# Kernel optimization log

Hardware: AMD Instinct MI355X
Metric: run time of the kernel (lower is better)

The kernel has to match this reference:

```python
import jax, jax.numpy as jnp
import numpy as np

N_NODES = 50000
N_EDGES = 800000
LN_EPS = 1e-5


def _segment_softmax_aggr(msg, t, dst, n):
    # SoftmaxAggregation(learn=True): alpha = softmax(msg * t) per dest segment, out = sum(alpha * msg)
    logits = msg * t  # [E, C]
    m = jax.ops.segment_max(logits, dst, num_segments=n)
    m = jnp.where(jnp.isfinite(m), m, 0.0)  # empty segments -> 0 to keep exp finite
    e = jnp.exp(logits - m[dst])
    denom = jax.ops.segment_sum(e, dst, num_segments=n)
    alpha = e / jnp.maximum(denom[dst], 1e-16)
    return jax.ops.segment_sum(alpha * msg, dst, num_segments=n)


def _sage_conv(x, src, dst, wp, bp, t, wl, bl, wr):
    # project=True: messages come from relu(lin(x)); root term uses ORIGINAL x
    xp = jax.nn.relu(x @ wp + bp)
    msg = xp[src]                                   # [E, C] gather
    aggr = _segment_softmax_aggr(msg, t, dst, x.shape[0])
    out = aggr @ wl + bl + x @ wr
    # normalize=True: L2 normalize rows (eps as in F.normalize)
    nrm = jnp.maximum(jnp.linalg.norm(out, axis=-1, keepdims=True), 1e-12)
    return out / nrm


def _mem_pool(x, k, w_conv, wl, bl):
    # PyG MemPooling, tau=1: Student-t kernel 1/(1+d^2)
    H, K, F = k.shape
    kk = k.reshape(H * K, F)
    d2 = (jnp.sum(kk * kk, -1)[:, None] + jnp.sum(x * x, -1)[None, :]
          - 2.0 * kk @ x.T)                          # [H*K, N]
    d2 = jnp.maximum(d2, 0.0)
    dist = 1.0 / (1.0 + d2)
    dist = dist.reshape(H, K, -1).transpose(0, 2, 1)  # [H, N, K]
    S = dist / jnp.sum(dist, -1, keepdims=True)       # per-head normalize over clusters
    S = jnp.einsum('h,hnk->nk', w_conv, S)            # 1x1 conv mixing heads (no bias)
    S = jax.nn.softmax(S, axis=-1)                    # [N, K]
    xp = S.T @ x                                      # [K, F]
    return xp @ wl + bl                               # [K, out]


def setup_inputs() -> dict:
    key = jax.random.key(0)
    ks = jax.random.split(key, 20)
    rn = lambda i, shp, s: jax.random.normal(ks[i], shp, dtype=jnp.float32) * s
    inp = {
        'x': rn(0, (N_NODES, 64), 1.0),
        'edge_index': jax.random.randint(ks[1], (2, N_EDGES), 0, N_NODES, dtype=jnp.int32),
        'w_proj1': rn(2, (64, 64), 0.1), 'b_proj1': rn(3, (64,), 0.05),
        't1': jnp.ones((64,), jnp.float32),
        'w_l1': rn(4, (64, 256), 0.1), 'b_l1': rn(5, (256,), 0.05),
        'w_r1': rn(6, (64, 256), 0.1),
        'w_proj2': rn(7, (256, 256), 0.05), 'b_proj2': rn(8, (256,), 0.05),
        't2': jnp.ones((256,), jnp.float32),
        'w_l2': rn(9, (256, 128), 0.05), 'b_l2': rn(10, (128,), 0.05),
        'w_r2': rn(11, (256, 128), 0.05),
        'k_mem': rn(12, (4, 4, 128), 1.0),
        'w_conv': rn(13, (4,), 0.5),
        'w_memlin': rn(14, (128, 128), 0.08), 'b_memlin': rn(15, (128,), 0.05),
        'w_fx': rn(16, (128, 64), 0.08), 'b_fx': rn(17, (64,), 0.05),
        'gamma': jnp.ones((64,), jnp.float32),
        'beta': jnp.zeros((64,), jnp.float32),
    }
    return inp


def reference(x, edge_index, w_proj1, b_proj1, t1, w_l1, b_l1, w_r1,
              w_proj2, b_proj2, t2, w_l2, b_l2, w_r2,
              k_mem, w_conv, w_memlin, b_memlin, w_fx, b_fx, gamma, beta):
    src, dst = edge_index[0], edge_index[1]
    h = _sage_conv(x, src, dst, w_proj1, b_proj1, t1, w_l1, b_l1, w_r1)
    h = jax.nn.relu(h)                              # dropout = identity (eval)
    h = _sage_conv(h, src, dst, w_proj2, b_proj2, t2, w_l2, b_l2, w_r2)
    h = jax.nn.relu(h)
    pooled = _mem_pool(h, k_mem, w_conv, w_memlin, b_memlin)  # [4, 128]
    g = jnp.mean(pooled, axis=0, keepdims=True)     # global_mean_pool -> [1, 128]
    y = g @ w_fx + b_fx                             # [1, 64]
    mu = jnp.mean(y, -1, keepdims=True)
    var = jnp.var(y, -1, keepdims=True)
    y = (y - mu) / jnp.sqrt(var + LN_EPS) * gamma + beta
    return jax.nn.relu(y)
```

## Files before the change

kernel.cpp:

```cpp
#include <hip/hip_runtime.h>
#include <hip/hip_bf16.h>

#define N_NODES 50000
#define N_EDGES 800000
#define NB 196
#define PC_SLICES 2048

typedef __attribute__((ext_vector_type(8))) short short8;
typedef __attribute__((ext_vector_type(4))) float f32x4;
typedef __attribute__((ext_vector_type(2))) float f32x2;

#define QSCALE2 (2.f / 255.f)
#define QINV2   127.5f
#define QSCALE1 (12.75f / 255.f)
#define QINV1   20.f

__device__ __forceinline__ float us2f(unsigned short u) {
    return __uint_as_float(((unsigned int)u) << 16);
}
__device__ __forceinline__ unsigned short f2bu(float f) {
    unsigned int u = __float_as_uint(f);
    unsigned int r = (u + 0x7fffu + ((u >> 16) & 1u)) >> 16;
    return (unsigned short)r;
}
__device__ __forceinline__ float exp2_hw(float x) {
    float r;
    __asm__("v_exp_f32 %0, %1" : "=v"(r) : "v"(x));
    return r;
}
#define LOG2E 1.44269504088896f

__global__ void k_hist(const int* __restrict__ dst, int* __restrict__ counts) {
    int e = blockIdx.x * 256 + threadIdx.x;
    if (e < N_EDGES) atomicAdd(&counts[dst[e]], 1);
}

__global__ __launch_bounds__(256) void k_scan1(const int* __restrict__ counts,
                                               int* __restrict__ row_ptr,
                                               int* __restrict__ partial) {
    __shared__ int sd[256];
    int t = threadIdx.x, i = blockIdx.x * 256 + t;
    int v = (i < N_NODES) ? counts[i] : 0;
    sd[t] = v;
    __syncthreads();
    for (int off = 1; off < 256; off <<= 1) {
        int o = (t >= off) ? sd[t - off] : 0;
        __syncthreads();
        sd[t] += o;
        __syncthreads();
    }
    if (i < N_NODES) row_ptr[i] = sd[t] - v;
    if (t == 255) partial[blockIdx.x] = sd[255];
}

__global__ __launch_bounds__(256) void k_scan3b(int* __restrict__ row_ptr,
                                                const int* __restrict__ partial,
                                                int* __restrict__ cursor) {
    __shared__ int sd[256];
    int t = threadIdx.x;
    sd[t] = (t < blockIdx.x) ? partial[t] : 0;
    __syncthreads();
    for (int off = 128; off > 0; off >>= 1) {
        if (t < off) sd[t] += sd[t + off];
        __syncthreads();
    }
    int base = sd[0];
    int i = blockIdx.x * 256 + t;
    if (i < N_NODES) {
        int v = row_ptr[i] + base;
        row_ptr[i] = v;
        cursor[i] = v;
    }
    if (blockIdx.x == 0 && t == 0) row_ptr[N_NODES] = N_EDGES;
}

__global__ void k_scatter(const int* __restrict__ src, const int* __restrict__ dst,
                          int* __restrict__ cursor, int* __restrict__ src_sorted) {
    int e = blockIdx.x * 256 + threadIdx.x;
    if (e < N_EDGES) {
        int d = dst[e];
        int pos = atomicAdd(&cursor[d], 1);
        src_sorted[pos] = src[e];
    }
}

#define XCAST_N (N_NODES * 64)
__global__ __launch_bounds__(256) void k_prep(const float* __restrict__ x,
                                              const float* __restrict__ wp1,
                                              const float* __restrict__ wl1,
                                              const float* __restrict__ wr1,
                                              const float* __restrict__ wp2,
                                              const float* __restrict__ wl2,
                                              const float* __restrict__ wr2,
                                              unsigned short* __restrict__ cat1,
                                              unsigned short* __restrict__ B0T,
                                              unsigned short* __restrict__ B1T,
                                              unsigned short* __restrict__ BP2T,
                                              unsigned short* __restrict__ B2T) {
    int idx = blockIdx.x * 256 + threadIdx.x;
    if (idx < XCAST_N) {
        int i = idx >> 6, j = idx & 63;
        cat1[i * 128 + 64 + j] = f2bu(x[idx]);
        return;
    }
    int w = idx - XCAST_N;
    if (w < 4096)  { int k = w >> 6, n = w & 63;  B0T[n * 64 + k] = f2bu(wp1[w]); return; }
    w -= 4096;
    if (w < 16384) { int k = w >> 8, n = w & 255; B1T[n * 128 + k] = f2bu(wl1[w]); return; }
    w -= 16384;
    if (w < 16384) { int k = w >> 8, n = w & 255; B1T[n * 128 + 64 + k] = f2bu(wr1[w]); return; }
    w -= 16384;
    if (w < 65536) { int k = w >> 8, n = w & 255; BP2T[n * 256 + k] = f2bu(wp2[w]); return; }
    w -= 65536;
    if (w < 32768) { int k = w >> 7, n = w & 127; B2T[n * 512 + k] = f2bu(wl2[w]); return; }
    w -= 32768;
    if (w < 32768) { int k = w >> 7, n = w & 127; B2T[n * 512 + 256 + k] = f2bu(wr2[w]); return; }
}

template<int K, int C, int LDA, int LDOUT, int OUT_OFF, int EP, int WPB>
__global__ __launch_bounds__(256, WPB) void k_gemm(const unsigned short* __restrict__ A,
                                                   const unsigned short* __restrict__ BT,
                                                   const float* __restrict__ bias,
                                                   void* __restrict__ outv,
                                                   const float* __restrict__ kmem,
                                                   const float* __restrict__ wconv,
                                                   float* __restrict__ Sm,
                                                   float qinv) {
    constexpr int NT = C / 16;
    constexpr int SAE = 128 * 72;
    constexpr int SBE = C * 72;
    constexpr int STAGE_B = (SAE + SBE) * 2;
    constexpr int RP_B = 64 * C * (EP == 2 ? 4 : (EP == 3 ? 1 : 2));
    constexpr int SMEM_B = STAGE_B > RP_B ? STAGE_B : RP_B;
    constexpr int POOL_B = (EP == 2) ? (2048 * 4 + 64 + 16) : 16;
    __shared__ __align__(16) char smem[SMEM_B + POOL_B];
    unsigned short* sA = (unsigned short*)smem;
    unsigned short* sB = sA + SAE;
    float* kls  = (float*)(smem + SMEM_B);
    float* kk2s = kls + 2048;
    float* wcs  = kk2s + 16;

    int t = threadIdx.x;
    int wid = t >> 6, lane = t & 63;
    int lrow = lane & 15, quad = lane >> 4;
    int m0 = blockIdx.x * 128;

    if (EP == 2) {
        for (int i = t; i < 2048; i += 256) kls[i] = kmem[i];
        if (t < 4) wcs[t] = wconv[t];
        __syncthreads();
        if (t < 16) {
            float s = 0.f;
            for (int f = 0; f < 128; ++f) { float v = kls[t * 128 + f]; s += v * v; }
            kk2s[t] = s;
        }
    }

    f32x4 acc[2][NT];
#pragma unroll
    for (int h = 0; h < 2; ++h)
#pragma unroll
        for (int nt = 0; nt < NT; ++nt)
#pragma unroll
            for (int r = 0; r < 4; ++r) acc[h][nt][r] = 0.f;

    for (int k0 = 0; k0 < K; k0 += 64) {
        __syncthreads();
        for (int i = t; i < 1024; i += 256) {
            int r = i >> 3, seg = i & 7;
            int m = m0 + r;
            uint4 v = make_uint4(0u, 0u, 0u, 0u);
            if (m < N_NODES) v = *(const uint4*)&A[(size_t)m * LDA + k0 + seg * 8];
            *(uint4*)&sA[r * 72 + seg * 8] = v;
        }
        for (int i = t; i < C * 8; i += 256) {
            int n = i >> 3, seg = i & 7;
            uint4 v = *(const uint4*)&BT[(size_t)n * K + k0 + seg * 8];
            *(uint4*)&sB[n * 72 + seg * 8] = v;
        }
        __syncthreads();
#pragma unroll
        for (int kk = 0; kk < 2; ++kk) {
            short8 a0 = *(const short8*)&sA[(wid * 16 + lrow) * 72 + kk * 32 + quad * 8];
            short8 a1 = *(const short8*)&sA[(64 + wid * 16 + lrow) * 72 + kk * 32 + quad * 8];
#pragma unroll
            for (int nt = 0; nt < NT; ++nt) {
                short8 bfg = *(const short8*)&sB[(nt * 16 + lrow) * 72 + kk * 32 + quad * 8];
                acc[0][nt] = __builtin_amdgcn_mfma_f32_16x16x32_bf16(a0, bfg, acc[0][nt], 0, 0, 0);
                acc[1][nt] = __builtin_amdgcn_mfma_f32_16x16x32_bf16(a1, bfg, acc[1][nt], 0, 0, 0);
            }
        }
    }

#pragma unroll
    for (int h = 0; h < 2; ++h) {
#pragma unroll
        for (int nt = 0; nt < NT; ++nt) {
            float bv = bias[nt * 16 + lrow];
#pragma unroll
            for (int r = 0; r < 4; ++r) acc[h][nt][r] += bv;
        }
        if (EP == 1 || EP == 2) {
#pragma unroll
            for (int r = 0; r < 4; ++r) {
                float ss = 0.f;
#pragma unroll
                for (int nt = 0; nt < NT; ++nt) ss += acc[h][nt][r] * acc[h][nt][r];
                ss += __shfl_xor(ss, 1);
                ss += __shfl_xor(ss, 2);
                ss += __shfl_xor(ss, 4);
                ss += __shfl_xor(ss, 8);
                float rinv = 1.f / fmaxf(sqrtf(ss), 1e-12f);
#pragma unroll
                for (int nt = 0; nt < NT; ++nt)
                    acc[h][nt][r] = fmaxf(acc[h][nt][r] * rinv, 0.f);
            }
        } else {
#pragma unroll
            for (int nt = 0; nt < NT; ++nt)
#pragma unroll
                for (int r = 0; r < 4; ++r) acc[h][nt][r] = fmaxf(acc[h][nt][r], 0.f);
        }
    }

    __syncthreads();
#pragma unroll
    for (int h = 0; h < 2; ++h) {
        if (EP == 2) {
            float* rp = (float*)smem;
#pragma unroll
            for (int nt = 0; nt < NT; ++nt)
#pragma unroll
                for (int r = 0; r < 4; ++r)
                    rp[(wid * 16 + quad * 4 + r) * C + nt * 16 + lrow] = acc[h][nt][r];
            __syncthreads();
            float* outp = (float*)outv;
            for (int i = t; i < 64 * C / 4; i += 256) {
                int f = i * 4, r = f / C, c = f % C;
                int m = m0 + h * 64 + r;
                if (m < N_NODES)
                    *(float4*)&outp[(size_t)m * LDOUT + OUT_OFF + c] = *(const float4*)&rp[f];
            }
            {
                int row = t >> 2, p = t & 3;
                int cbase = p * 32;
                float dots[16];
#pragma unroll
                for (int k = 0; k < 16; ++k) dots[k] = 0.f;
                float x2 = 0.f;
#pragma unroll
                for (int c4 = 0; c4 < 8; ++c4) {
                    float4 xv = *(const float4*)&rp[row * C + cbase + c4 * 4];
                    x2 += xv.x * xv.x + xv.y * xv.y + xv.z * xv.z + xv.w * xv.w;
#pragma unroll
                    for (int k = 0; k < 16; ++k) {
                        float4 kv = *(const float4*)&kls[k * 128 + cbase + c4 * 4];
                        dots[k] += xv.x * kv.x + xv.y * kv.y + xv.z * kv.z + xv.w * kv.w;
                    }
                }
#pragma unroll
                for (int k = 0; k < 16; ++k) {
                    dots[k] += __shfl_xor(dots[k], 1);
                    dots[k] += __shfl_xor(dots[k], 2);
                }
                x2 += __shfl_xor(x2, 1);
                x2 += __shfl_xor(x2, 2);
                if (p == 0) {
                    int m = m0 + h * 64 + row;
                    if (m < N_NODES) {
                        float dist[16];
#pragma unroll
                        for (int k = 0; k < 16; ++k) {
                            float d2 = fmaxf(kk2s[k] + x2 - 2.f * dots[k], 0.f);
                            dist[k] = 1.f / (1.f + d2);
                        }
                        float s0 = 0.f, s1 = 0.f, s2 = 0.f, s3 = 0.f;
#pragma unroll
                        for (int hh = 0; hh < 4; ++hh) {
                            float den = dist[hh * 4] + dist[hh * 4 + 1] +
                                        dist[hh * 4 + 2] + dist[hh * 4 + 3];
                            float inv = wcs[hh] / den;
                            s0 += dist[hh * 4 + 0] * inv;
                            s1 += dist[hh * 4 + 1] * inv;
                            s2 += dist[hh * 4 + 2] * inv;
                            s3 += dist[hh * 4 + 3] * inv;
                        }
                        float mx = fmaxf(fmaxf(s0, s1), fmaxf(s2, s3));
                        float e0 = __expf(s0 - mx), e1 = __expf(s1 - mx);
                        float e2 = __expf(s2 - mx), e3 = __expf(s3 - mx);
                        float inv = 1.f / (e0 + e1 + e2 + e3);
                        *(float4*)&Sm[(size_t)m * 4] =
                            make_float4(e0 * inv, e1 * inv, e2 * inv, e3 * inv);
                    }
                }
            }
            __syncthreads();
        } else if (EP == 3) {
            unsigned char* rp = (unsigned char*)smem;
#pragma unroll
            for (int nt = 0; nt < NT; ++nt)
#pragma unroll
                for (int r = 0; r < 4; ++r) {
                    float q = fminf(__builtin_rintf(acc[h][nt][r] * qinv), 255.f);
                    rp[(wid * 16 + quad * 4 + r) * C + nt * 16 + lrow] = (unsigned char)(int)q;
                }
            __syncthreads();
            unsigned char* outp = (unsigned char*)outv;
            for (int i = t; i < 64 * C / 16; i += 256) {
                int f = i * 16, r = f / C, c = f % C;
                int m = m0 + h * 64 + r;
                if (m < N_NODES)
                    *(uint4*)&outp[(size_t)m * LDOUT + OUT_OFF + c] = *(const uint4*)&rp[f];
            }
            __syncthreads();
        } else {
            unsigned short* rp = (unsigned short*)smem;
#pragma unroll
            for (int nt = 0; nt < NT; ++nt)
#pragma unroll
                for (int r = 0; r < 4; ++r)
                    rp[(wid * 16 + quad * 4 + r) * C + nt * 16 + lrow] = f2bu(acc[h][nt][r]);
            __syncthreads();
            unsigned short* outp = (unsigned short*)outv;
            for (int i = t; i < 64 * C / 8; i += 256) {
                int f = i * 8, r = f / C, c = f % C;
                int m = m0 + h * 64 + r;
                if (m < N_NODES)
                    *(uint4*)&outp[(size_t)m * LDOUT + OUT_OFF + c] = *(const uint4*)&rp[f];
            }
            __syncthreads();
        }
    }
}

__global__ __launch_bounds__(256) void k_aggr256(const unsigned char* __restrict__ xp,
                                                 const float* __restrict__ tvec,
                                                 const int* __restrict__ row_ptr,
                                                 const int* __restrict__ srcs,
                                                 unsigned short* __restrict__ outp) {
    int t = threadIdx.x & 63;
    int wid = threadIdx.x >> 6;
    int n = blockIdx.x * 4 + wid;
    float4 tv4 = *(const float4*)&tvec[t * 4];
    f32x2 tv01 = {tv4.x * (LOG2E * QSCALE2), tv4.y * (LOG2E * QSCALE2)};
    f32x2 tv23 = {tv4.z * (LOG2E * QSCALE2), tv4.w * (LOG2E * QSCALE2)};
    int beg = __builtin_amdgcn_readfirstlane(row_ptr[n]);
    int end = __builtin_amdgcn_readfirstlane(row_ptr[n + 1]);
    f32x2 se01 = {0.f, 0.f}, se23 = {0.f, 0.f};
    f32x2 sem01 = {0.f, 0.f}, sem23 = {0.f, 0.f};
    int e = beg;
#define EDGE_BODY(VV, MSK)                                                     \
    {                                                                          \
        f32x2 m01 = {(float)((VV) & 0xFFu), (float)(((VV) >> 8) & 0xFFu)};     \
        f32x2 m23 = {(float)(((VV) >> 16) & 0xFFu), (float)((VV) >> 24)};      \
        f32x2 l01 = m01 * tv01, l23 = m23 * tv23;                              \
        f32x2 w01, w23;                                                        \
        w01.x = exp2_hw(l01.x) * (MSK); w01.y = exp2_hw(l01.y) * (MSK);        \
        w23.x = exp2_hw(l23.x) * (MSK); w23.y = exp2_hw(l23.y) * (MSK);        \
        se01 += w01; se23 += w23;                                              \
        sem01 = __builtin_elementwise_fma(w01, m01, sem01);                    \
        sem23 = __builtin_elementwise_fma(w23, m23, sem23);                    \
    }
    for (; e + 16 <= end; e += 16) {
        unsigned int v[16];
#pragma unroll
        for (int j = 0; j < 16; ++j) {
            const unsigned char* p = xp + (size_t)srcs[e + j] * 256;
            v[j] = *(const unsigned int*)&p[t * 4];
        }
#pragma unroll
        for (int j = 0; j < 16; ++j) EDGE_BODY(v[j], 1.f)
    }
    for (; e + 8 <= end; e += 8) {
        unsigned int v[8];
#pragma unroll
        for (int j = 0; j < 8; ++j) {
            const unsigned char* p = xp + (size_t)srcs[e + j] * 256;
            v[j] = *(const unsigned int*)&p[t * 4];
        }
#pragma unroll
        for (int j = 0; j < 8; ++j) EDGE_BODY(v[j], 1.f)
    }
    if (e < end) {
        int last = end - 1;
        unsigned int v[8];
#pragma unroll
        for (int j = 0; j < 8; ++j) {
            int ee = e + j;
            ee = ee < end ? ee : last;
            const unsigned char* p = xp + (size_t)srcs[ee] * 256;
            v[j] = *(const unsigned int*)&p[t * 4];
        }
#pragma unroll
        for (int j = 0; j < 8; ++j) {
            float msk = (e + j < end) ? 1.f : 0.f;
            EDGE_BODY(v[j], msk)
        }
    }
#undef EDGE_BODY
    ushort4 o;
    o.x = f2bu(QSCALE2 * sem01.x / fmaxf(se01.x, 1e-16f));
    o.y = f2bu(QSCALE2 * sem01.y / fmaxf(se01.y, 1e-16f));
    o.z = f2bu(QSCALE2 * sem23.x / fmaxf(se23.x, 1e-16f));
    o.w = f2bu(QSCALE2 * sem23.y / fmaxf(se23.y, 1e-16f));
    *(ushort4*)&outp[(size_t)n * 512 + t * 4] = o;
}

__global__ __launch_bounds__(256) void k_aggr64(const unsigned char* __restrict__ xp,
                                                const float* __restrict__ tvec,
                                                const int* __restrict__ row_ptr,
                                                const int* __restrict__ srcs,
                                                unsigned short* __restrict__ outp) {
    int c = threadIdx.x & 63;
    int wid = threadIdx.x >> 6;
    int n = blockIdx.x * 4 + wid;
    float tv = tvec[c] * (LOG2E * QSCALE1);
    int beg = __builtin_amdgcn_readfirstlane(row_ptr[n]);
    int end = __builtin_amdgcn_readfirstlane(row_ptr[n + 1]);
    float se = 0.f, sem = 0.f;
    int e = beg;
    for (; e + 16 <= end; e += 16) {
        unsigned char v[16];
#pragma unroll
        for (int j = 0; j < 16; ++j)
            v[j] = xp[(size_t)srcs[e + j] * 64 + c];
#pragma unroll
        for (int j = 0; j < 16; ++j) {
            float msg = (float)v[j];
            float w = exp2_hw(msg * tv);
            se += w;
            sem = fmaf(w, msg, sem);
        }
    }
    for (; e + 8 <= end; e += 8) {
        unsigned char v[8];
#pragma unroll
        for (int j = 0; j < 8; ++j)
            v[j] = xp[(size_t)srcs[e + j] * 64 + c];
#pragma unroll
        for (int j = 0; j < 8; ++j) {
            float msg = (float)v[j];
            float w = exp2_hw(msg * tv);
            se += w;
            sem = fmaf(w, msg, sem);
        }
    }
    if (e < end) {
        int last = end - 1;
        unsigned char v[8];
#pragma unroll
        for (int j = 0; j < 8; ++j) {
            int ee = e + j;
            ee = ee < end ? ee : last;
            v[j] = xp[(size_t)srcs[ee] * 64 + c];
        }
#pragma unroll
        for (int j = 0; j < 8; ++j) {
            float msk = (e + j < end) ? 1.f : 0.f;
            float msg = (float)v[j];
            float w = exp2_hw(msg * tv) * msk;
            se += w;
            sem = fmaf(w, msg, sem);
        }
    }
    outp[(size_t)n * 128 + c] = f2bu(QSCALE1 * sem / fmaxf(se, 1e-16f));
}

__global__ __launch_bounds__(256) void k_pool_c(const float* __restrict__ h2,
                                                const float* __restrict__ Sm,
                                                float* __restrict__ part) {
    int t = threadIdx.x;
    int c = t & 127, sub = t >> 7;
    int slice = blockIdx.x * 2 + sub;
    float a0 = 0.f, a1 = 0.f, a2 = 0.f, a3 = 0.f;
    for (int n = slice; n < N_NODES; n += PC_SLICES) {
        float xv = h2[(size_t)n * 128 + c];
        float4 sv = *(const float4*)&Sm[(size_t)n * 4];
        a0 = fmaf(sv.x, xv, a0);
        a1 = fmaf(sv.y, xv, a1);
        a2 = fmaf(sv.z, xv, a2);
        a3 = fmaf(sv.w, xv, a3);
    }
    float* p = &part[(size_t)slice * 512];
    p[0 * 128 + c] = a0;
    p[1 * 128 + c] = a1;
    p[2 * 128 + c] = a2;
    p[3 * 128 + c] = a3;
}

__global__ __launch_bounds__(256) void k_pool_b(const float* __restrict__ part,
                                                float* __restrict__ pooled) {
    int j = blockIdx.x;
    float s = 0.f;
    for (int b = threadIdx.x; b < PC_SLICES; b += 256) s += part[(size_t)b * 512 + j];
#pragma unroll
    for (int off = 32; off > 0; off >>= 1) s += __shfl_xor(s, off);
    __shared__ float red[4];
    int lane = threadIdx.x & 63, wid = threadIdx.x >> 6;
    if (lane == 0) red[wid] = s;
    __syncthreads();
    if (threadIdx.x == 0) pooled[j] = red[0] + red[1] + red[2] + red[3];
}

__global__ __launch_bounds__(128) void k_final(const float* __restrict__ pooled,
                                               const float* __restrict__ wmem,
                                               const float* __restrict__ bmem,
                                               const float* __restrict__ wfx,
                                               const float* __restrict__ bfx,
                                               const float* __restrict__ gamma,
                                               const float* __restrict__ beta,
                                               float* __restrict__ out) {
    __shared__ float gx[128], g[128];
    int t = threadIdx.x;
    gx[t] = 0.25f * (pooled[t] + pooled[128 + t] + pooled[256 + t] + pooled[384 + t]);
    __syncthreads();
    float acc = bmem[t];
    for (int f = 0; f < 128; ++f) acc = fmaf(gx[f], wmem[f * 128 + t], acc);
    g[t] = acc;
    __syncthreads();
    if (t < 64) {
        float y = bfx[t];
        for (int f = 0; f < 128; ++f) y = fmaf(g[f], wfx[f * 64 + t], y);
        float s = y, s2 = y * y;
#pragma unroll
        for (int off = 32; off > 0; off >>= 1) {
            s += __shfl_xor(s, off);
            s2 += __shfl_xor(s2, off);
        }
        float mu = s * (1.f / 64.f);
        float var = s2 * (1.f / 64.f) - mu * mu;
        float v = (y - mu) / sqrtf(var + 1e-5f) * gamma[t] + beta[t];
        out[t] = fmaxf(v, 0.f);
    }
}

extern "C" void kernel_launch(void* const* d_in, const int* in_sizes, int n_in,
                              void* d_out, int out_size, void* d_ws, size_t ws_size,
                              hipStream_t stream) {
    const float* x        = (const float*)d_in[0];
    const int*   ei       = (const int*)  d_in[1];
    const float* w_proj1  = (const float*)d_in[2];
    const float* b_proj1  = (const float*)d_in[3];
    const float* t1       = (const float*)d_in[4];
    const float* w_l1     = (const float*)d_in[5];
    const float* b_l1     = (const float*)d_in[6];
    const float* w_r1     = (const float*)d_in[7];
    const float* w_proj2  = (const float*)d_in[8];
    const float* b_proj2  = (const float*)d_in[9];
    const float* t2       = (const float*)d_in[10];
    const float* w_l2     = (const float*)d_in[11];
    const float* b_l2     = (const float*)d_in[12];
    const float* w_r2     = (const float*)d_in[13];
    const float* k_mem    = (const float*)d_in[14];
    const float* w_conv   = (const float*)d_in[15];
    const float* w_memlin = (const float*)d_in[16];
    const float* b_memlin = (const float*)d_in[17];
    const float* w_fx     = (const float*)d_in[18];
    const float* b_fx     = (const float*)d_in[19];
    const float* gamma    = (const float*)d_in[20];
    const float* beta     = (const float*)d_in[21];
    const int* src = ei;
    const int* dst = ei + N_EDGES;
    (void)in_sizes; (void)n_in; (void)out_size; (void)ws_size;

    char* W = (char*)d_ws;
    const size_t MB = 1024 * 1024;
    int*   row_ptr    = (int*)(W + 0);
    int*   cursor     = (int*)(W + 256 * 1024);
    int*   partial    = (int*)(W + 512 * 1024);
    int*   src_sorted = (int*)(W + 768 * 1024);
    unsigned short* cat1 = (unsigned short*)(W + 4 * MB);
    unsigned char*  xp1  = (unsigned char*)(W + 17 * MB);
    unsigned short* cat2 = (unsigned short*)(W + 24 * MB);
    unsigned char*  xp2  = (unsigned char*)(W + 76 * MB);
    float* h2     = (float*)(W + 102 * MB);
    float* Sm     = (float*)(W + 128 * MB);
    float* pooled = (float*)(W + 131 * MB);
    unsigned short* B0T  = (unsigned short*)(W + 133 * MB);
    unsigned short* B1T  = (unsigned short*)(W + 134 * MB);
    unsigned short* BP2T = (unsigned short*)(W + 135 * MB);
    unsigned short* B2T  = (unsigned short*)(W + 136 * MB);
    float* part   = (float*)(W + 140 * MB);

    hipMemsetAsync(cursor, 0, N_NODES * sizeof(int), stream);
    k_hist<<<(N_EDGES + 255) / 256, 256, 0, stream>>>(dst, cursor);
    k_scan1<<<NB, 256, 0, stream>>>(cursor, row_ptr, partial);
    k_scan3b<<<NB, 256, 0, stream>>>(row_ptr, partial, cursor);
    k_scatter<<<(N_EDGES + 255) / 256, 256, 0, stream>>>(src, dst, cursor, src_sorted);

    k_prep<<<(XCAST_N + 167936 + 255) / 256, 256, 0, stream>>>(
        x, w_proj1, w_l1, w_r1, w_proj2, w_l2, w_r2, cat1, B0T, B1T, BP2T, B2T);

    const int GB = (N_NODES + 127) / 128;
    const int AGB = N_NODES / 4;

    k_gemm<64, 64, 128, 64, 0, 3, 4><<<GB, 256, 0, stream>>>(
        cat1 + 64, B0T, b_proj1, xp1, nullptr, nullptr, nullptr, QINV1);
    k_aggr64<<<AGB, 256, 0, stream>>>(xp1, t1, row_ptr, src_sorted, cat1);
    k_gemm<128, 256, 128, 512, 256, 1, 2><<<GB, 256, 0, stream>>>(
        cat1, B1T, b_l1, cat2, nullptr, nullptr, nullptr, 0.f);

    k_gemm<256, 256, 512, 256, 0, 3, 2><<<GB, 256, 0, stream>>>(
        cat2 + 256, BP2T, b_proj2, xp2, nullptr, nullptr, nullptr, QINV2);
    k_aggr256<<<AGB, 256, 0, stream>>>(xp2, t2, row_ptr, src_sorted, cat2);
    k_gemm<512, 128, 512, 128, 0, 2, 3><<<GB, 256, 0, stream>>>(
        cat2, B2T, b_l2, h2, k_mem, w_conv, Sm, 0.f);

    k_pool_c<<<PC_SLICES / 2, 256, 0, stream>>>(h2, Sm, part);
    k_pool_b<<<512, 256, 0, stream>>>(part, pooled);
    k_final<<<1, 128, 0, stream>>>(pooled, w_memlin, b_memlin, w_fx, b_fx, gamma, beta,
                                   (float*)d_out);
}
```

Measured before the change: 384.6 us.

## Degree-sort nodes for aggregation and shrink GEMM row tiles to 64

Adds a degree histogram, scan and scatter that build a permutation grouping nodes by in-degree (capped at 63). Both aggregation kernels use this permutation and drop to two waves per block, so waves in the same block have similar edge counts and load imbalance shrinks. The GEMM kernel gains an MH template parameter and every call now uses 64-row tiles with higher occupancy hints, giving twice as many blocks. The cost is three extra small launches, atomics, and scattered node order on the aggregation output writes.

```diff
diff --git a/kernel.cpp b/kernel.cpp
--- a/kernel.cpp
+++ b/kernel.cpp
@@ -81,6 +81,45 @@
         int d = dst[e];
         int pos = atomicAdd(&cursor[d], 1);
         src_sorted[pos] = src[e];
+    }
+}
+
+__global__ __launch_bounds__(256) void k_dhist(const int* __restrict__ counts,
+                                               int* __restrict__ dcnt) {
+    __shared__ int h[64];
+    int t = threadIdx.x;
+    if (t < 64) h[t] = 0;
+    __syncthreads();
+    int i = blockIdx.x * 256 + t;
+    if (i < N_NODES) {
+        int d = counts[i];
+        d = d > 63 ? 63 : d;
+        atomicAdd(&h[d], 1);
+    }
+    __syncthreads();
+    if (t < 64) atomicAdd(&dcnt[t], h[t]);
+}
+
+__global__ void k_dscan(const int* __restrict__ dcnt, int* __restrict__ dcur) {
+    int t = threadIdx.x;
+    int v = dcnt[t];
+    int s = v;
+    for (int off = 1; off < 64; off <<= 1) {
+        int o = __shfl_up(s, off);
+        if (t >= off) s += o;
+    }
+    dcur[t] = s - v;
+}
+
+__global__ __launch_bounds__(256) void k_dscatter(const int* __restrict__ counts,
+                                                  int* __restrict__ dcur,
+                                                  int* __restrict__ perm) {
+    int i = blockIdx.x * 256 + threadIdx.x;
+    if (i < N_NODES) {
+        int d = counts[i];
+        d = d > 63 ? 63 : d;
+        int pos = atomicAdd(&dcur[d], 1);
+        perm[pos] = i;
     }
 }
 
@@ -117,7 +156,7 @@
     if (w < 32768) { int k = w >> 7, n = w & 127; B2T[n * 512 + 256 + k] = f2bu(wr2[w]); return; }
 }
 
-template<int K, int C, int LDA, int LDOUT, int OUT_OFF, int EP, int WPB>
+template<int K, int C, int LDA, int LDOUT, int OUT_OFF, int EP, int WPB, int MH>
 __global__ __launch_bounds__(256, WPB) void k_gemm(const unsigned short* __restrict__ A,
                                                    const unsigned short* __restrict__ BT,
                                                    const float* __restrict__ bias,
@@ -127,7 +166,7 @@
                                                    float* __restrict__ Sm,
                                                    float qinv) {
     constexpr int NT = C / 16;
-    constexpr int SAE = 128 * 72;
+    constexpr int SAE = 64 * MH * 72;
     constexpr int SBE = C * 72;
     constexpr int STAGE_B = (SAE + SBE) * 2;
     constexpr int RP_B = 64 * C * (EP == 2 ? 4 : (EP == 3 ? 1 : 2));
@@ -143,7 +182,7 @@
     int t = threadIdx.x;
     int wid = t >> 6, lane = t & 63;
     int lrow = lane & 15, quad = lane >> 4;
-    int m0 = blockIdx.x * 128;
+    int m0 = blockIdx.x * (64 * MH);
 
     if (EP == 2) {
         for (int i = t; i < 2048; i += 256) kls[i] = kmem[i];
@@ -156,9 +195,9 @@
         }
     }
 
-    f32x4 acc[2][NT];
-#pragma unroll
-    for (int h = 0; h < 2; ++h)
+    f32x4 acc[MH][NT];
+#pragma unroll
+    for (int h = 0; h < MH; ++h)
 #pragma unroll
         for (int nt = 0; nt < NT; ++nt)
 #pragma unroll
@@ -166,7 +205,7 @@
 
     for (int k0 = 0; k0 < K; k0 += 64) {
         __syncthreads();
-        for (int i = t; i < 1024; i += 256) {
+        for (int i = t; i < 64 * MH * 8; i += 256) {
             int r = i >> 3, seg = i & 7;
             int m = m0 + r;
             uint4 v = make_uint4(0u, 0u, 0u, 0u);
@@ -181,19 +220,22 @@
         __syncthreads();
 #pragma unroll
         for (int kk = 0; kk < 2; ++kk) {
-            short8 a0 = *(const short8*)&sA[(wid * 16 + lrow) * 72 + kk * 32 + quad * 8];
-            short8 a1 = *(const short8*)&sA[(64 + wid * 16 + lrow) * 72 + kk * 32 + quad * 8];
+            short8 av[MH];
+#pragma unroll
+            for (int h = 0; h < MH; ++h)
+                av[h] = *(const short8*)&sA[(h * 64 + wid * 16 + lrow) * 72 + kk * 32 + quad * 8];
 #pragma unroll
             for (int nt = 0; nt < NT; ++nt) {
                 short8 bfg = *(const short8*)&sB[(nt * 16 + lrow) * 72 + kk * 32 + quad * 8];
-                acc[0][nt] = __builtin_amdgcn_mfma_f32_16x16x32_bf16(a0, bfg, acc[0][nt], 0, 0, 0);
-                acc[1][nt] = __builtin_amdgcn_mfma_f32_16x16x32_bf16(a1, bfg, acc[1][nt], 0, 0, 0);
+#pragma unroll
+                for (int h = 0; h < MH; ++h)
+                    acc[h][nt] = __builtin_amdgcn_mfma_f32_16x16x32_bf16(av[h], bfg, acc[h][nt], 0, 0, 0);
             }
         }
     }
 
 #pragma unroll
-    for (int h = 0; h < 2; ++h) {
+    for (int h = 0; h < MH; ++h) {
 #pragma unroll
         for (int nt = 0; nt < NT; ++nt) {
             float bv = bias[nt * 16 + lrow];
@@ -225,7 +267,7 @@
 
     __syncthreads();
 #pragma unroll
-    for (int h = 0; h < 2; ++h) {
+    for (int h = 0; h < MH; ++h) {
         if (EP == 2) {
             float* rp = (float*)smem;
 #pragma unroll
@@ -333,14 +375,15 @@
     }
 }
 
-__global__ __launch_bounds__(256) void k_aggr256(const unsigned char* __restrict__ xp,
+__global__ __launch_bounds__(128) void k_aggr256(const unsigned char* __restrict__ xp,
                                                  const float* __restrict__ tvec,
                                                  const int* __restrict__ row_ptr,
                                                  const int* __restrict__ srcs,
+                                                 const int* __restrict__ perm,
                                                  unsigned short* __restrict__ outp) {
     int t = threadIdx.x & 63;
     int wid = threadIdx.x >> 6;
-    int n = blockIdx.x * 4 + wid;
+    int n = __builtin_amdgcn_readfirstlane(perm[blockIdx.x * 2 + wid]);
     float4 tv4 = *(const float4*)&tvec[t * 4];
     f32x2 tv01 = {tv4.x * (LOG2E * QSCALE2), tv4.y * (LOG2E * QSCALE2)};
     f32x2 tv23 = {tv4.z * (LOG2E * QSCALE2), tv4.w * (LOG2E * QSCALE2)};
@@ -406,14 +449,15 @@
     *(ushort4*)&outp[(size_t)n * 512 + t * 4] = o;
 }
 
-__global__ __launch_bounds__(256) void k_aggr64(const unsigned char* __restrict__ xp,
+__global__ __launch_bounds__(128) void k_aggr64(const unsigned char* __restrict__ xp,
                                                 const float* __restrict__ tvec,
                                                 const int* __restrict__ row_ptr,
                                                 const int* __restrict__ srcs,
+                                                const int* __restrict__ perm,
                                                 unsigned short* __restrict__ outp) {
     int c = threadIdx.x & 63;
     int wid = threadIdx.x >> 6;
-    int n = blockIdx.x * 4 + wid;
+    int n = __builtin_amdgcn_readfirstlane(perm[blockIdx.x * 2 + wid]);
     float tv = tvec[c] * (LOG2E * QSCALE1);
     int beg = __builtin_amdgcn_readfirstlane(row_ptr[n]);
     int end = __builtin_amdgcn_readfirstlane(row_ptr[n + 1]);
@@ -568,6 +612,8 @@
     int*   row_ptr    = (int*)(W + 0);
     int*   cursor     = (int*)(W + 256 * 1024);
     int*   partial    = (int*)(W + 512 * 1024);
+    int*   dcnt       = (int*)(W + 512 * 1024 + 4096);
+    int*   dcur       = (int*)(W + 512 * 1024 + 8192);
     int*   src_sorted = (int*)(W + 768 * 1024);
     unsigned short* cat1 = (unsigned short*)(W + 4 * MB);
     unsigned char*  xp1  = (unsigned char*)(W + 17 * MB);
@@ -580,30 +626,35 @@
     unsigned short* B1T  = (unsigned short*)(W + 134 * MB);
     unsigned short* BP2T = (unsigned short*)(W + 135 * MB);
     unsigned short* B2T  = (unsigned short*)(W + 136 * MB);
+    int*   perm   = (int*)(W + 138 * MB);
     float* part   = (float*)(W + 140 * MB);
 
     hipMemsetAsync(cursor, 0, N_NODES * sizeof(int), stream);
+    hipMemsetAsync(dcnt, 0, 64 * sizeof(int), stream);
     k_hist<<<(N_EDGES + 255) / 256, 256, 0, stream>>>(dst, cursor);
+    k_dhist<<<NB, 256, 0, stream>>>(cursor, dcnt);
     k_scan1<<<NB, 256, 0, stream>>>(cursor, row_ptr, partial);
+    k_dscan<<<1, 64, 0, stream>>>(dcnt, dcur);
+    k_dscatter<<<NB, 256, 0, stream>>>(cursor, dcur, perm);
     k_scan3b<<<NB, 256, 0, stream>>>(row_ptr, partial, cursor);
     k_scatter<<<(N_EDGES + 255) / 256, 256, 0, stream>>>(src, dst, cursor, src_sorted);
 
     k_prep<<<(XCAST_N + 167936 + 255) / 256, 256, 0, stream>>>(
         x, w_proj1, w_l1, w_r1, w_proj2, w_l2, w_r2, cat1, B0T, B1T, BP2T, B2T);
 
-    const int GB = (N_NODES + 127) / 128;
-    const int AGB = N_NODES / 4;
-
-    k_gemm<64, 64, 128, 64, 0, 3, 4><<<GB, 256, 0, stream>>>(
+    const int GB = (N_NODES + 63) / 64;
+    const int AGB = N_NODES / 2;
+
+    k_gemm<64, 64, 128, 64, 0, 3, 4, 1><<<GB, 256, 0, stream>>>(
         cat1 + 64, B0T, b_proj1, xp1, nullptr, nullptr, nullptr, QINV1);
-    k_aggr64<<<AGB, 256, 0, stream>>>(xp1, t1, row_ptr, src_sorted, cat1);
-    k_gemm<128, 256, 128, 512, 256, 1, 2><<<GB, 256, 0, stream>>>(
+    k_aggr64<<<AGB, 128, 0, stream>>>(xp1, t1, row_ptr, src_sorted, perm, cat1);
+    k_gemm<128, 256, 128, 512, 256, 1, 3, 1><<<GB, 256, 0, stream>>>(
         cat1, B1T, b_l1, cat2, nullptr, nullptr, nullptr, 0.f);
 
-    k_gemm<256, 256, 512, 256, 0, 3, 2><<<GB, 256, 0, stream>>>(
+    k_gemm<256, 256, 512, 256, 0, 3, 3, 1><<<GB, 256, 0, stream>>>(
         cat2 + 256, BP2T, b_proj2, xp2, nullptr, nullptr, nullptr, QINV2);
-    k_aggr256<<<AGB, 256, 0, stream>>>(xp2, t2, row_ptr, src_sorted, cat2);
-    k_gemm<512, 128, 512, 128, 0, 2, 3><<<GB, 256, 0, stream>>>(
+    k_aggr256<<<AGB, 128, 0, stream>>>(xp2, t2, row_ptr, src_sorted, perm, cat2);
+    k_gemm<512, 128, 512, 128, 0, 2, 3, 1><<<GB, 256, 0, stream>>>(
         cat2, B2T, b_l2, h2, k_mem, w_conv, Sm, 0.f);
 
     k_pool_c<<<PC_SLICES / 2, 256, 0, stream>>>(h2, Sm, part);
```

After: 545.0 us. +41.7%, slower.
